# Optimization experiments

Measured on AMD Instinct MI355X. Metric: run time of the kernel, lower is better.

Reference implementation:

```python
import jax, jax.numpy as jnp
import numpy as np

EPS = 1e-5
GROUPS = 32
NH = 4


def group_norm(x, gamma, beta, groups=GROUPS, eps=EPS):
    # x: (B, C, H, W); normalize over (C//groups, H, W) per group
    B, C, H, W = x.shape
    xg = x.reshape(B, groups, C // groups, H, W)
    mean = xg.mean(axis=(2, 3, 4), keepdims=True)
    var = xg.var(axis=(2, 3, 4), keepdims=True)
    xn = ((xg - mean) * jax.lax.rsqrt(var + eps)).reshape(B, C, H, W)
    return xn * gamma[None, :, None, None] + beta[None, :, None, None]


def conv1x1(x, w, b):
    # x: (B, Cin, H, W), w: (Cout, Cin), b: (Cout,)
    return jnp.einsum('bchw,oc->bohw', x, w) + b[None, :, None, None]


def setup_inputs() -> dict:
    key = jax.random.key(0)
    ks = jax.random.split(key, 16)
    B, C, H, W = 4, 256, 64, 64
    d = {}
    d['x'] = jax.random.normal(ks[0], (B, C, H, W), jnp.float32)
    d['cond'] = jax.random.normal(ks[1], (B, C, H, W), jnp.float32)
    s = 1.0 / np.sqrt(C)
    d['gn_q_w'] = jnp.ones((C,), jnp.float32)
    d['gn_q_b'] = jnp.zeros((C,), jnp.float32)
    d['gn_kv_w'] = jnp.ones((C,), jnp.float32)
    d['gn_kv_b'] = jnp.zeros((C,), jnp.float32)
    d['wq'] = jax.random.normal(ks[2], (C, C), jnp.float32) * s
    d['bq'] = jnp.zeros((C,), jnp.float32)
    d['wk'] = jax.random.normal(ks[3], (C, C), jnp.float32) * s
    d['bk'] = jnp.zeros((C,), jnp.float32)
    d['wv'] = jax.random.normal(ks[4], (C, C), jnp.float32) * s
    d['bv'] = jnp.zeros((C,), jnp.float32)
    d['wo'] = jax.random.normal(ks[5], (C, C), jnp.float32) * s
    d['bo'] = jnp.zeros((C,), jnp.float32)
    return d


def reference(x, cond, gn_q_w, gn_q_b, gn_kv_w, gn_kv_b,
              wq, bq, wk, bk, wv, bv, wo, bo):
    B, C, H, W = x.shape
    hd = C // NH
    N = H * W
    scale = hd ** -0.5
    kv_in = group_norm(cond, gn_kv_w, gn_kv_b)
    q = conv1x1(group_norm(x, gn_q_w, gn_q_b), wq, bq)
    k = conv1x1(kv_in, wk, bk)
    v = conv1x1(kv_in, wv, bv)
    # (B, nh, head_dim, N) layout as in the original
    q = q.reshape(B, NH, hd, N)
    k = k.reshape(B, NH, hd, N)
    v = v.reshape(B, NH, hd, N)
    attn = jnp.einsum('bhdn,bhdm->bhnm', q, k) * scale
    attn = jax.nn.softmax(attn, axis=-1)
    out = jnp.einsum('bhnm,bhdm->bhdn', attn, v).reshape(B, C, H, W)
    return x + conv1x1(out, wo, bo)
```

## Files before the change

### kernel.cpp

```cpp
#include <hip/hip_runtime.h>
#include <hip/hip_bf16.h>

#define B_   4
#define C_   256
#define N_   4096
#define NH_  4
#define HD_  64
#define G_   32
#define CPG_ 8
#define EPS_ 1e-5f

typedef __bf16 bf16x8 __attribute__((ext_vector_type(8)));
typedef __bf16 bf16x4 __attribute__((ext_vector_type(4)));
typedef float  f32x4  __attribute__((ext_vector_type(4)));
typedef unsigned int u32x4 __attribute__((ext_vector_type(4)));
typedef unsigned int u32x2 __attribute__((ext_vector_type(2)));

#define EXP2F(x) __builtin_amdgcn_exp2f(x)

static __device__ __forceinline__ unsigned int packbf(float a, float b) {
    __bf16 x = (__bf16)a, y = (__bf16)b;
    unsigned short ux = __builtin_bit_cast(unsigned short, x);
    unsigned short uy = __builtin_bit_cast(unsigned short, y);
    return (unsigned int)ux | ((unsigned int)uy << 16);
}

__global__ __launch_bounds__(256) void wconv_kernel(const float* __restrict__ w0,
                                                    const float* __restrict__ w1,
                                                    const float* __restrict__ w2,
                                                    const float* __restrict__ w3,
                                                    __bf16* __restrict__ dst) {
    const float* srcs[4] = {w0, w1, w2, w3};
    const float* s = srcs[blockIdx.y];
    __bf16* d = dst + (size_t)blockIdx.y * C_ * C_;
    const int i = blockIdx.x * 256 + threadIdx.x;
    float4 v = ((const float4*)s)[i];
    bf16x4 o;
    o[0] = (__bf16)v.x; o[1] = (__bf16)v.y; o[2] = (__bf16)v.z; o[3] = (__bf16)v.w;
    ((bf16x4*)d)[i] = o;
}

__global__ __launch_bounds__(256) void gn_kernel(const float* __restrict__ in,
                                                 const float* __restrict__ gw,
                                                 const float* __restrict__ gb,
                                                 __bf16* __restrict__ out) {
    const int b = blockIdx.x / G_;
    const int g = blockIdx.x % G_;
    const int tid = threadIdx.x;
    const size_t base = ((size_t)b * C_ + g * CPG_) * N_;
    const float4* pv = (const float4*)(in + base);
    const int NC = (CPG_ * N_) / 4;

    float s = 0.f, ss = 0.f;
    for (int i = tid; i < NC; i += 256) {
        float4 v = pv[i];
        s  += v.x + v.y + v.z + v.w;
        ss += v.x * v.x + v.y * v.y + v.z * v.z + v.w * v.w;
    }
    #pragma unroll
    for (int m = 32; m >= 1; m >>= 1) { s += __shfl_xor(s, m); ss += __shfl_xor(ss, m); }
    __shared__ float red[8];
    const int w = tid >> 6;
    if ((tid & 63) == 0) { red[w] = s; red[4 + w] = ss; }
    __syncthreads();
    s  = red[0] + red[1] + red[2] + red[3];
    ss = red[4] + red[5] + red[6] + red[7];
    const float mean = s * (1.f / 32768.f);
    const float var  = ss * (1.f / 32768.f) - mean * mean;
    const float rinv = rsqrtf(var + EPS_);

    float sc[CPG_], sh[CPG_];
    #pragma unroll
    for (int j = 0; j < CPG_; j++) {
        const float gm = gw[g * CPG_ + j], bt = gb[g * CPG_ + j];
        sc[j] = rinv * gm;
        sh[j] = bt - mean * rinv * gm;
    }
    __bf16* ob = out + (size_t)b * N_ * C_ + g * CPG_;
    for (int n = tid; n < N_; n += 256) {
        bf16x8 o;
        #pragma unroll
        for (int j = 0; j < CPG_; j++) {
            const float v = in[base + (size_t)j * N_ + n];
            o[j] = (__bf16)(v * sc[j] + sh[j]);
        }
        *(bf16x8*)(ob + (size_t)n * C_) = o;
    }
}

__global__ __launch_bounds__(256) void qkv_kernel(const __bf16* __restrict__ Wall,
                                                  const float* __restrict__ bq,
                                                  const float* __restrict__ bk,
                                                  const float* __restrict__ bv,
                                                  const __bf16* __restrict__ Xq,
                                                  const __bf16* __restrict__ Xkv,
                                                  __bf16* __restrict__ Qo,
                                                  __bf16* __restrict__ Ko,
                                                  __bf16* __restrict__ Vo,
                                                  float qscale) {
    const int n0 = blockIdx.x * 64;
    const int sel = blockIdx.y >> 1;
    const int m0 = (blockIdx.y & 1) * 128;
    const int b  = blockIdx.z;
    const int tid = threadIdx.x;
    const int w = tid >> 6, lane = tid & 63, quad = lane >> 4, l16 = lane & 15;
    const int wn = (w >> 1) * 32;
    const int wm = (w & 1) * 64;

    const __bf16* Wb   = Wall + (size_t)sel * C_ * C_;
    const __bf16* XT   = (sel == 0) ? Xq : Xkv;
    const float*  bias = (sel == 0) ? bq : ((sel == 1) ? bk : bv);
    const float   psc  = (sel == 0) ? qscale : 1.0f;

    __shared__ union {
        __bf16 Wl[128][264];
        __bf16 T1[64][136];
    } sm;

    const __bf16* wsrc = Wb + (size_t)m0 * C_;
    #pragma unroll
    for (int i = 0; i < 16; i++) {
        const int e = i * 256 + tid;
        const int row = e >> 5;
        const int c8 = (e & 31) * 8;
        *(bf16x8*)(&sm.Wl[row][c8]) = *(const bf16x8*)(wsrc + (size_t)row * C_ + c8);
    }

    const __bf16* ap0 = XT + ((size_t)b * N_ + n0 + wn + l16) * C_ + quad * 8;
    const __bf16* ap1 = ap0 + (size_t)16 * C_;
    bf16x8 areg[2][8];
    #pragma unroll
    for (int ks = 0; ks < 8; ks++) {
        areg[0][ks] = *(const bf16x8*)(ap0 + ks * 32);
        areg[1][ks] = *(const bf16x8*)(ap1 + ks * 32);
    }

    f32x4 acc[2][4];
    #pragma unroll
    for (int qg = 0; qg < 2; qg++)
        #pragma unroll
        for (int jm = 0; jm < 4; jm++) acc[qg][jm] = (f32x4){0.f, 0.f, 0.f, 0.f};

    __syncthreads();

    #pragma unroll
    for (int ks = 0; ks < 8; ks++) {
        const int kc = ks * 32;
        #pragma unroll
        for (int jm = 0; jm < 4; jm++) {
            bf16x8 bw = *(const bf16x8*)(&sm.Wl[wm + jm * 16 + l16][kc + quad * 8]);
            acc[0][jm] = __builtin_amdgcn_mfma_f32_16x16x32_bf16(areg[0][ks], bw, acc[0][jm], 0, 0, 0);
            acc[1][jm] = __builtin_amdgcn_mfma_f32_16x16x32_bf16(areg[1][ks], bw, acc[1][jm], 0, 0, 0);
        }
    }

    if (sel == 2) {
        #pragma unroll
        for (int qg = 0; qg < 2; qg++) {
            const int nn = n0 + wn + qg * 16 + quad * 4;
            #pragma unroll
            for (int jm = 0; jm < 4; jm++) {
                const int m = m0 + wm + jm * 16 + l16;
                const float bi = bias[m];
                bf16x4 o;
                #pragma unroll
                for (int r = 0; r < 4; r++) o[r] = (__bf16)(acc[qg][jm][r] + bi);
                *(bf16x4*)(Vo + (size_t)(b * C_ + m) * N_ + nn) = o;
            }
        }
    } else {
        __bf16* OUTb = (sel == 0) ? Qo : Ko;
        __syncthreads();
        #pragma unroll
        for (int qg = 0; qg < 2; qg++)
            #pragma unroll
            for (int jm = 0; jm < 4; jm++) {
                const int m = m0 + wm + jm * 16 + l16;
                const float bi = bias[m];
                #pragma unroll
                for (int r = 0; r < 4; r++)
                    sm.T1[wn + qg * 16 + quad * 4 + r][wm + jm * 16 + l16] =
                        (__bf16)((acc[qg][jm][r] + bi) * psc);
            }
        __syncthreads();
        const int h0 = m0 >> 6;
        #pragma unroll
        for (int i = 0; i < 4; i++) {
            const int idx = i * 256 + tid;
            const int row = idx >> 4;
            const int c = (idx & 15) * 8;
            const int hh = h0 + (c >> 6);
            const int d = c & 63;
            *(bf16x8*)(OUTb + ((size_t)(b * NH_ + hh) * N_ + n0 + row) * HD_ + d) =
                *(const bf16x8*)(&sm.T1[row][c]);
        }
    }
}

__global__ __launch_bounds__(256) void gemm_kernel(const __bf16* __restrict__ Wb,
                                                   const float* __restrict__ bias,
                                                   const __bf16* __restrict__ XT,
                                                   float* __restrict__ OUTf,
                                                   const float* __restrict__ RES) {
    const int n0 = blockIdx.x * 64;
    const int m0 = blockIdx.y * 128;
    const int b  = blockIdx.z;
    const int tid = threadIdx.x;
    const int w = tid >> 6, lane = tid & 63, quad = lane >> 4, l16 = lane & 15;
    const int wn = (w >> 1) * 32;
    const int wm = (w & 1) * 64;

    __shared__ __bf16 Wl[128][264];

    const __bf16* wsrc = Wb + (size_t)m0 * C_;
    #pragma unroll
    for (int i = 0; i < 16; i++) {
        const int e = i * 256 + tid;
        const int row = e >> 5;
        const int c8 = (e & 31) * 8;
        *(bf16x8*)(&Wl[row][c8]) = *(const bf16x8*)(wsrc + (size_t)row * C_ + c8);
    }

    const __bf16* ap0 = XT + ((size_t)b * N_ + n0 + wn + l16) * C_ + quad * 8;
    const __bf16* ap1 = ap0 + (size_t)16 * C_;
    bf16x8 areg[2][8];
    #pragma unroll
    for (int ks = 0; ks < 8; ks++) {
        areg[0][ks] = *(const bf16x8*)(ap0 + ks * 32);
        areg[1][ks] = *(const bf16x8*)(ap1 + ks * 32);
    }

    f32x4 acc[2][4];
    #pragma unroll
    for (int qg = 0; qg < 2; qg++)
        #pragma unroll
        for (int jm = 0; jm < 4; jm++) acc[qg][jm] = (f32x4){0.f, 0.f, 0.f, 0.f};

    __syncthreads();

    #pragma unroll
    for (int ks = 0; ks < 8; ks++) {
        const int kc = ks * 32;
        #pragma unroll
        for (int jm = 0; jm < 4; jm++) {
            bf16x8 bw = *(const bf16x8*)(&Wl[wm + jm * 16 + l16][kc + quad * 8]);
            acc[0][jm] = __builtin_amdgcn_mfma_f32_16x16x32_bf16(areg[0][ks], bw, acc[0][jm], 0, 0, 0);
            acc[1][jm] = __builtin_amdgcn_mfma_f32_16x16x32_bf16(areg[1][ks], bw, acc[1][jm], 0, 0, 0);
        }
    }

    #pragma unroll
    for (int qg = 0; qg < 2; qg++) {
        const int nn = n0 + wn + qg * 16 + quad * 4;
        #pragma unroll
        for (int jm = 0; jm < 4; jm++) {
            const int m = m0 + wm + jm * 16 + l16;
            const float bi = bias[m];
            const size_t off = (size_t)(b * C_ + m) * N_ + nn;
            const float4 res = *(const float4*)(RES + off);
            f32x4 v;
            v[0] = acc[qg][jm][0] + bi + res.x;
            v[1] = acc[qg][jm][1] + bi + res.y;
            v[2] = acc[qg][jm][2] + bi + res.z;
            v[3] = acc[qg][jm][3] + bi + res.w;
            *(f32x4*)(OUTf + off) = v;
        }
    }
}

__global__ __launch_bounds__(256, 2) void attn_kernel(const __bf16* __restrict__ qT,
                                                      const __bf16* __restrict__ kT,
                                                      const __bf16* __restrict__ V,
                                                      __bf16* __restrict__ O) {
    const int flat = blockIdx.y * 32 + blockIdx.x;
    const int bh = flat & 15;
    const int qt = flat >> 4;
    const int q0 = qt * 128;
    const int b = bh >> 2, h = bh & 3;
    const int tid = threadIdx.x;
    const int w = tid >> 6, lane = tid & 63, quad = lane >> 4, l16 = lane & 15;

    __shared__ union SMem {
        struct { __bf16 K[2][64][72]; __bf16 Vt[2][64][72]; } kv;
        __bf16 Ot[128][72];
    } sm;

    const __bf16* qTb = qT + (size_t)bh * N_ * HD_;
    const __bf16* kTb = kT + (size_t)bh * N_ * HD_;
    const __bf16* Vb  = V + ((size_t)b * C_ + h * HD_) * N_;

    bf16x8 qa[2][2];
    #pragma unroll
    for (int qg = 0; qg < 2; qg++)
        #pragma unroll
        for (int kk = 0; kk < 2; kk++)
            qa[qg][kk] = *(const bf16x8*)(qTb + (size_t)(q0 + w * 32 + qg * 16 + l16) * HD_ + kk * 32 + quad * 8);

    f32x4 oacc[2][4];
    #pragma unroll
    for (int qg = 0; qg < 2; qg++)
        #pragma unroll
        for (int j = 0; j < 4; j++) oacc[qg][j] = (f32x4){0.f, 0.f, 0.f, 0.f};
    float lsum[2] = {0.f, 0.f};

    const int srow = tid >> 3;
    const int scol = (tid & 7) * 8;

    bf16x8 rk[2], rv[2];
    #pragma unroll
    for (int i = 0; i < 2; i++) {
        const int row = srow + i * 32;
        rk[i] = *(const bf16x8*)(kTb + (size_t)row * HD_ + scol);
        rv[i] = *(const bf16x8*)(Vb + (size_t)row * N_ + scol);
    }

    for (int it = 0; it < N_ / 64; it++) {
        const int cur = it & 1;
        const int nm0 = ((it + 1) * 64) & (N_ - 1);
        #pragma unroll
        for (int i = 0; i < 2; i++) {
            const int row = srow + i * 32;
            *(bf16x8*)(&sm.kv.K[cur][row][scol])  = rk[i];
            *(bf16x8*)(&sm.kv.Vt[cur][row][scol]) = rv[i];
        }
        #pragma unroll
        for (int i = 0; i < 2; i++) {
            const int row = srow + i * 32;
            rk[i] = *(const bf16x8*)(kTb + (size_t)(nm0 + row) * HD_ + scol);
            rv[i] = *(const bf16x8*)(Vb + (size_t)row * N_ + nm0 + scol);
        }
        __syncthreads();
        bf16x8 kb[2][4], vb[2][4];
        #pragma unroll
        for (int kk = 0; kk < 2; kk++)
            #pragma unroll
            for (int j = 0; j < 4; j++) {
                kb[kk][j] = *(const bf16x8*)(&sm.kv.K[cur][j * 16 + l16][kk * 32 + quad * 8]);
                vb[kk][j] = *(const bf16x8*)(&sm.kv.Vt[cur][j * 16 + l16][kk * 32 + quad * 8]);
            }
        #pragma unroll
        for (int qg = 0; qg < 2; qg++) {
            f32x4 s[4];
            #pragma unroll
            for (int j = 0; j < 4; j++) s[j] = (f32x4){0.f, 0.f, 0.f, 0.f};
            #pragma unroll
            for (int kk = 0; kk < 2; kk++)
                #pragma unroll
                for (int j = 0; j < 4; j++)
                    s[j] = __builtin_amdgcn_mfma_f32_16x16x32_bf16(kb[kk][j], qa[qg][kk], s[j], 0, 0, 0);
            float p[4][4];
            float ls = 0.f;
            #pragma unroll
            for (int j = 0; j < 4; j++) {
                #pragma unroll
                for (int r = 0; r < 4; r++) p[j][r] = EXP2F(s[j][r]);
                ls += (p[j][0] + p[j][1]) + (p[j][2] + p[j][3]);
            }
            lsum[qg] += ls;
            unsigned int pk0[4], pk1[4];
            #pragma unroll
            for (int j = 0; j < 4; j++) {
                pk0[j] = packbf(p[j][0], p[j][1]);
                pk1[j] = packbf(p[j][2], p[j][3]);
            }
            #pragma unroll
            for (int kk = 0; kk < 2; kk++) {
                u32x2 t0 = __builtin_amdgcn_permlane32_swap(pk0[2 * kk], pk0[2 * kk + 1], false, false);
                u32x2 t1 = __builtin_amdgcn_permlane32_swap(pk1[2 * kk], pk1[2 * kk + 1], false, false);
                u32x2 a0 = __builtin_amdgcn_permlane16_swap(t0[0], t0[1], false, false);
                u32x2 a1 = __builtin_amdgcn_permlane16_swap(t1[0], t1[1], false, false);
                bf16x8 pb = __builtin_bit_cast(bf16x8, (u32x4){a0[0], a1[0], a0[1], a1[1]});
                #pragma unroll
                for (int jd = 0; jd < 4; jd++)
                    oacc[qg][jd] = __builtin_amdgcn_mfma_f32_16x16x32_bf16(vb[kk][jd], pb, oacc[qg][jd], 0, 0, 0);
            }
        }
    }
    float inv[2];
    #pragma unroll
    for (int qg = 0; qg < 2; qg++) {
        float l = lsum[qg];
        l += __shfl_xor(l, 16);
        l += __shfl_xor(l, 32);
        inv[qg] = 1.f / l;
    }
    __syncthreads();
    #pragma unroll
    for (int qg = 0; qg < 2; qg++) {
        #pragma unroll
        for (int jd = 0; jd < 4; jd++) {
            bf16x4 o;
            #pragma unroll
            for (int r = 0; r < 4; r++) o[r] = (__bf16)(oacc[qg][jd][r] * inv[qg]);
            *(bf16x4*)(&sm.Ot[w * 32 + qg * 16 + l16][jd * 16 + quad * 4]) = o;
        }
    }
    __syncthreads();
    __bf16* Ob = O + ((size_t)b * N_ + q0) * C_ + h * HD_;
    const int row0 = tid >> 3, chh = (tid & 7) * 8;
    #pragma unroll
    for (int i = 0; i < 4; i++) {
        const int row = row0 + i * 32;
        *(bf16x8*)(Ob + (size_t)row * C_ + chh) = *(const bf16x8*)(&sm.Ot[row][chh]);
    }
}

extern "C" void kernel_launch(void* const* d_in, const int* in_sizes, int n_in,
                              void* d_out, int out_size, void* d_ws, size_t ws_size,
                              hipStream_t stream) {
    const float* x     = (const float*)d_in[0];
    const float* cond  = (const float*)d_in[1];
    const float* gnqw  = (const float*)d_in[2];
    const float* gnqb  = (const float*)d_in[3];
    const float* gnkw  = (const float*)d_in[4];
    const float* gnkb  = (const float*)d_in[5];
    const float* wq    = (const float*)d_in[6];
    const float* bq    = (const float*)d_in[7];
    const float* wk    = (const float*)d_in[8];
    const float* bk    = (const float*)d_in[9];
    const float* wv    = (const float*)d_in[10];
    const float* bv    = (const float*)d_in[11];
    const float* wo    = (const float*)d_in[12];
    const float* bo    = (const float*)d_in[13];
    float* out = (float*)d_out;

    const size_t TEN = (size_t)B_ * C_ * N_;
    __bf16* gnx   = (__bf16*)d_ws;
    __bf16* gnc   = gnx + TEN;
    __bf16* qT    = gnc + TEN;
    __bf16* kT    = qT  + TEN;
    __bf16* v     = kT  + TEN;
    __bf16* attno = v   + TEN;
    __bf16* wb    = attno + TEN;

    wconv_kernel<<<dim3(64, 4), 256, 0, stream>>>(wq, wk, wv, wo, wb);

    gn_kernel<<<dim3(B_ * G_), 256, 0, stream>>>(x,    gnqw, gnqb, gnx);
    gn_kernel<<<dim3(B_ * G_), 256, 0, stream>>>(cond, gnkw, gnkb, gnc);

    const size_t WSZ = (size_t)C_ * C_;
    qkv_kernel<<<dim3(N_ / 64, 6, B_), 256, 0, stream>>>(wb, bq, bk, bv, gnx, gnc,
                                                         qT, kT, v,
                                                         0.125f * 1.44269504088896f);

    attn_kernel<<<dim3(32, 16), 256, 0, stream>>>(qT, kT, v, attno);

    gemm_kernel<<<dim3(N_ / 64, C_ / 128, B_), 256, 0, stream>>>(wb + 3 * WSZ, bo, attno, out, x);
}
```

Before: 267.2 us.

## Split group norm into stats and tiled transpose kernels; stage GEMM epilogues through LDS

Group norm is split into a stats kernel and a normalize kernel. The stats kernel covers both inputs in one launch. The normalize kernel uses many more blocks and transposes channel-major data to token-major through a swizzled LDS tile, so stores are coalesced. The V epilogue of the QKV kernel and the output-projection epilogue now go through shared memory, so global writes and residual reads become wide and coalesced rather than strided 4-element accesses. The cost is an extra kernel launch, a second full read of the inputs, and extra LDS traffic and barriers.

```diff
diff --git a/kernel.cpp b/kernel.cpp
--- a/kernel.cpp
+++ b/kernel.cpp
@@ -40,10 +40,17 @@
     ((bf16x4*)d)[i] = o;
 }
 
-__global__ __launch_bounds__(256) void gn_kernel(const float* __restrict__ in,
-                                                 const float* __restrict__ gw,
-                                                 const float* __restrict__ gb,
-                                                 __bf16* __restrict__ out) {
+__global__ __launch_bounds__(256) void gn_stats_kernel(const float* __restrict__ in0,
+                                                       const float* __restrict__ in1,
+                                                       const float* __restrict__ gw0,
+                                                       const float* __restrict__ gb0,
+                                                       const float* __restrict__ gw1,
+                                                       const float* __restrict__ gb1,
+                                                       float* __restrict__ stat) {
+    const int which = blockIdx.y;
+    const float* in = which ? in1 : in0;
+    const float* gw = which ? gw1 : gw0;
+    const float* gb = which ? gb1 : gb0;
     const int b = blockIdx.x / G_;
     const int g = blockIdx.x % G_;
     const int tid = threadIdx.x;
@@ -68,23 +75,48 @@
     const float mean = s * (1.f / 32768.f);
     const float var  = ss * (1.f / 32768.f) - mean * mean;
     const float rinv = rsqrtf(var + EPS_);
-
-    float sc[CPG_], sh[CPG_];
-    #pragma unroll
-    for (int j = 0; j < CPG_; j++) {
-        const float gm = gw[g * CPG_ + j], bt = gb[g * CPG_ + j];
-        sc[j] = rinv * gm;
-        sh[j] = bt - mean * rinv * gm;
-    }
-    __bf16* ob = out + (size_t)b * N_ * C_ + g * CPG_;
-    for (int n = tid; n < N_; n += 256) {
-        bf16x8 o;
-        #pragma unroll
-        for (int j = 0; j < CPG_; j++) {
-            const float v = in[base + (size_t)j * N_ + n];
-            o[j] = (__bf16)(v * sc[j] + sh[j]);
-        }
-        *(bf16x8*)(ob + (size_t)n * C_) = o;
+    if (tid < CPG_) {
+        const int c = g * CPG_ + tid;
+        float* sp = stat + (size_t)which * 2 * B_ * C_;
+        const float sc = rinv * gw[c];
+        sp[b * C_ + c] = sc;
+        sp[B_ * C_ + b * C_ + c] = gb[c] - mean * sc;
+    }
+}
+
+__global__ __launch_bounds__(256) void gn_norm_kernel(const float* __restrict__ in0,
+                                                      const float* __restrict__ in1,
+                                                      const float* __restrict__ stat,
+                                                      __bf16* __restrict__ out0,
+                                                      __bf16* __restrict__ out1) {
+    const int which = blockIdx.z;
+    const float* in = which ? in1 : in0;
+    __bf16* out = which ? out1 : out0;
+    const int n0 = blockIdx.x * 64;
+    const int b  = blockIdx.y;
+    const int tid = threadIdx.x;
+    const int w = tid >> 6, lane = tid & 63;
+    const float* scp = stat + (size_t)which * 2 * B_ * C_ + b * C_;
+    const float* shp = scp + B_ * C_;
+
+    __shared__ __bf16 Lt[64][264];
+
+    #pragma unroll 16
+    for (int p = 0; p < 64; p++) {
+        const int c = p * 4 + w;
+        const float v = in[((size_t)(b * C_ + c)) * N_ + n0 + lane];
+        const float o = v * scp[c] + shp[c];
+        const int ch = (((c >> 3) ^ (lane >> 3)) << 3) + (c & 7);
+        Lt[lane][ch] = (__bf16)o;
+    }
+    __syncthreads();
+    #pragma unroll
+    for (int q = 0; q < 8; q++) {
+        const int r = q * 8 + (tid >> 5);
+        const int l = tid & 31;
+        const int ch = (l ^ (r >> 3)) << 3;
+        *(bf16x8*)(out + ((size_t)b * N_ + n0 + r) * C_ + l * 8) =
+            *(const bf16x8*)(&Lt[r][ch]);
     }
 }
 
@@ -115,6 +147,7 @@
     __shared__ union {
         __bf16 Wl[128][264];
         __bf16 T1[64][136];
+        __bf16 Tv[128][72];
     } sm;
 
     const __bf16* wsrc = Wb + (size_t)m0 * C_;
@@ -155,18 +188,26 @@
     }
 
     if (sel == 2) {
-        #pragma unroll
-        for (int qg = 0; qg < 2; qg++) {
-            const int nn = n0 + wn + qg * 16 + quad * 4;
+        __syncthreads();
+        #pragma unroll
+        for (int qg = 0; qg < 2; qg++)
             #pragma unroll
             for (int jm = 0; jm < 4; jm++) {
-                const int m = m0 + wm + jm * 16 + l16;
-                const float bi = bias[m];
+                const int mm = wm + jm * 16 + l16;
+                const int nn = wn + qg * 16 + quad * 4;
+                const float bi = bias[m0 + mm];
                 bf16x4 o;
                 #pragma unroll
                 for (int r = 0; r < 4; r++) o[r] = (__bf16)(acc[qg][jm][r] + bi);
-                *(bf16x4*)(Vo + (size_t)(b * C_ + m) * N_ + nn) = o;
+                *(bf16x4*)(&sm.Tv[mm][nn]) = o;
             }
+        __syncthreads();
+        #pragma unroll
+        for (int i = 0; i < 4; i++) {
+            const int mrow = i * 32 + (tid >> 3);
+            const int ch = (tid & 7) * 8;
+            *(bf16x8*)(Vo + (size_t)(b * C_ + m0 + mrow) * N_ + n0 + ch) =
+                *(const bf16x8*)(&sm.Tv[mrow][ch]);
         }
     } else {
         __bf16* OUTb = (sel == 0) ? Qo : Ko;
@@ -210,7 +251,10 @@
     const int wn = (w >> 1) * 32;
     const int wm = (w & 1) * 64;
 
-    __shared__ __bf16 Wl[128][264];
+    __shared__ union {
+        __bf16 Wl[128][264];
+        float  Tf[128][68];
+    } sm;
 
     const __bf16* wsrc = Wb + (size_t)m0 * C_;
     #pragma unroll
@@ -218,7 +262,7 @@
         const int e = i * 256 + tid;
         const int row = e >> 5;
         const int c8 = (e & 31) * 8;
-        *(bf16x8*)(&Wl[row][c8]) = *(const bf16x8*)(wsrc + (size_t)row * C_ + c8);
+        *(bf16x8*)(&sm.Wl[row][c8]) = *(const bf16x8*)(wsrc + (size_t)row * C_ + c8);
     }
 
     const __bf16* ap0 = XT + ((size_t)b * N_ + n0 + wn + l16) * C_ + quad * 8;
@@ -243,28 +287,35 @@
         const int kc = ks * 32;
         #pragma unroll
         for (int jm = 0; jm < 4; jm++) {
-            bf16x8 bw = *(const bf16x8*)(&Wl[wm + jm * 16 + l16][kc + quad * 8]);
+            bf16x8 bw = *(const bf16x8*)(&sm.Wl[wm + jm * 16 + l16][kc + quad * 8]);
             acc[0][jm] = __builtin_amdgcn_mfma_f32_16x16x32_bf16(areg[0][ks], bw, acc[0][jm], 0, 0, 0);
             acc[1][jm] = __builtin_amdgcn_mfma_f32_16x16x32_bf16(areg[1][ks], bw, acc[1][jm], 0, 0, 0);
         }
     }
 
-    #pragma unroll
-    for (int qg = 0; qg < 2; qg++) {
-        const int nn = n0 + wn + qg * 16 + quad * 4;
+    __syncthreads();
+    #pragma unroll
+    for (int qg = 0; qg < 2; qg++)
         #pragma unroll
         for (int jm = 0; jm < 4; jm++) {
-            const int m = m0 + wm + jm * 16 + l16;
-            const float bi = bias[m];
-            const size_t off = (size_t)(b * C_ + m) * N_ + nn;
-            const float4 res = *(const float4*)(RES + off);
-            f32x4 v;
-            v[0] = acc[qg][jm][0] + bi + res.x;
-            v[1] = acc[qg][jm][1] + bi + res.y;
-            v[2] = acc[qg][jm][2] + bi + res.z;
-            v[3] = acc[qg][jm][3] + bi + res.w;
-            *(f32x4*)(OUTf + off) = v;
-        }
+            const int mm = wm + jm * 16 + l16;
+            const int nn = wn + qg * 16 + quad * 4;
+            const float bi = bias[m0 + mm];
+            f32x4 o;
+            #pragma unroll
+            for (int r = 0; r < 4; r++) o[r] = acc[qg][jm][r] + bi;
+            *(f32x4*)(&sm.Tf[mm][nn]) = o;
+        }
+    __syncthreads();
+    #pragma unroll
+    for (int qp = 0; qp < 8; qp++) {
+        const int mrow = qp * 16 + (tid >> 4);
+        const int k4 = (tid & 15) * 4;
+        const size_t off = (size_t)(b * C_ + m0 + mrow) * N_ + n0 + k4;
+        const float4 res = *(const float4*)(RES + off);
+        f32x4 v = *(const f32x4*)(&sm.Tf[mrow][k4]);
+        v[0] += res.x; v[1] += res.y; v[2] += res.z; v[3] += res.w;
+        *(f32x4*)(OUTf + off) = v;
     }
 }
 
@@ -425,6 +476,7 @@
     float* out = (float*)d_out;
 
     const size_t TEN = (size_t)B_ * C_ * N_;
+    const size_t WSZ = (size_t)C_ * C_;
     __bf16* gnx   = (__bf16*)d_ws;
     __bf16* gnc   = gnx + TEN;
     __bf16* qT    = gnc + TEN;
@@ -432,13 +484,13 @@
     __bf16* v     = kT  + TEN;
     __bf16* attno = v   + TEN;
     __bf16* wb    = attno + TEN;
+    float*  stat  = (float*)(wb + 4 * WSZ);
 
     wconv_kernel<<<dim3(64, 4), 256, 0, stream>>>(wq, wk, wv, wo, wb);
 
-    gn_kernel<<<dim3(B_ * G_), 256, 0, stream>>>(x,    gnqw, gnqb, gnx);
-    gn_kernel<<<dim3(B_ * G_), 256, 0, stream>>>(cond, gnkw, gnkb, gnc);
-
-    const size_t WSZ = (size_t)C_ * C_;
+    gn_stats_kernel<<<dim3(B_ * G_, 2), 256, 0, stream>>>(x, cond, gnqw, gnqb, gnkw, gnkb, stat);
+    gn_norm_kernel<<<dim3(N_ / 64, B_, 2), 256, 0, stream>>>(x, cond, stat, gnx, gnc);
+
     qkv_kernel<<<dim3(N_ / 64, 6, B_), 256, 0, stream>>>(wb, bq, bk, bv, gnx, gnc,
                                                          qT, kT, v,
                                                          0.125f * 1.44269504088896f);
```

After: 251.1 us. 1.06x faster.
